# Performance work log

Measured on AMD Instinct MI355X. Metric: run time of the kernel, lower is better.

The kernel has to match this reference:

```python
import jax, jax.numpy as jnp
import numpy as np

N, D, C = 8192, 128, 64
LAMBDA = 0.25
DELTA = 1.0


def setup_inputs() -> dict:
    key = jax.random.key(0)
    k1, k2, k3 = jax.random.split(key, 3)
    out = jax.random.normal(k1, (N, C), dtype=jnp.float32)
    feat = jax.random.normal(k2, (N, D), dtype=jnp.float32)
    y = jax.random.randint(k3, (N,), 0, C)
    return {"out": out, "feat": feat, "y": y}


def reference(out, feat, y):
    n = feat.shape[0]
    # Per-class matrices: zeroing rows not in class c leaves singular values
    # identical to slicing X[y==c] (extra zero rows only add zero singular
    # directions), so one batched SVD over [C, N, D] replaces the CPU loop.
    masks = (y[None, :] == jnp.arange(C)[:, None]).astype(feat.dtype)  # [C, N]
    Xc = feat[None, :, :] * masks[:, :, None]                           # [C, N, D]
    Sc = jnp.linalg.svd(Xc, compute_uv=False)                           # [C, min(N,D)]
    obj_c = jnp.maximum(Sc.sum(-1), DELTA).sum()                        # sum_c max(||X_c||_*, DELTA)
    S_all = jnp.linalg.svd(feat, compute_uv=False)
    ole = (obj_c - S_all.sum()) / n * LAMBDA
    # Cross entropy (mean reduction, matching nn.CrossEntropyLoss)
    logp = jax.nn.log_softmax(out, axis=-1)
    xe = -jnp.take_along_axis(logp, y[:, None], axis=1).mean()
    loss = ole + xe
    return jnp.reshape(loss, (1,))  # torch returns shape-[1] tensor
```

## Files before the change

### kernel.cpp

```cpp
#include <hip/hip_runtime.h>
#include <math.h>


#define N_ROWS 8192
#define DIM    128
#define NCLS   64
#define NITER  7
#define EPSN   2e-4f
#define LAMBDA_ 0.25f
#define DELTA_  1.0f
#define MAGIC  0x13579BDF

typedef __attribute__((ext_vector_type(8))) short s16x8;
typedef __attribute__((ext_vector_type(4))) short s16x4;
typedef __attribute__((ext_vector_type(4))) float f32x4;

static __device__ const float NS_C1[NITER] =
  {2.554408f, 2.491084f, 2.189178f, 2.050122f, 1.686417f, 1.5f, 1.5f};
static __device__ const float NS_C2[NITER] =
  {2.469261f, 2.290137f, 1.554316f, 1.276543f, 0.710544f, 0.5f, 0.5f};

__device__ __forceinline__ unsigned short f2bf(float f) {
  unsigned u = __float_as_uint(f);
  u = (u + 0x7FFFu + ((u >> 16) & 1u)) >> 16;
  return (unsigned short)u;
}
__device__ __forceinline__ float bf2f(unsigned short h) {
  return __uint_as_float(((unsigned)h) << 16);
}

__device__ __forceinline__ int swz_idx(int i, int j) {
  return i * 128 + (((j >> 3) ^ (i & 15)) << 3) + (j & 7);
}

__device__ __forceinline__ s16x8 load_frag(const short* buf, int row0,
                                           int kstep, int lane) {
  int m  = row0 + (lane & 15);
  int kg = kstep * 4 + (lane >> 4);
  return *(const s16x8*)(buf + m * 128 + ((kg ^ (m & 15)) << 3));
}

__device__ __forceinline__ void flag_set(int* p) {
  __threadfence();
  __hip_atomic_store(p, MAGIC, __ATOMIC_RELEASE, __HIP_MEMORY_SCOPE_AGENT);
}
__device__ __forceinline__ void flag_wait(const int* p) {
  while (__hip_atomic_load(p, __ATOMIC_ACQUIRE, __HIP_MEMORY_SCOPE_AGENT) != MAGIC)
    __builtin_amdgcn_s_sleep(8);
}

__global__ __launch_bounds__(512, 1) void ole_fused(const float* __restrict__ feat,
                                                    const int* __restrict__ y,
                                                    const float* __restrict__ logits,
                                                    float* __restrict__ Gall,
                                                    float* __restrict__ nuc,
                                                    float* __restrict__ cepart,
                                                    int* __restrict__ flags,
                                                    float* __restrict__ out) {
  int* gramdone = flags;
  int* nflag    = flags + NCLS;
  int* ceflag   = flags + 2 * NCLS;

  __shared__ __align__(16) short Yb[DIM * DIM];
  __shared__ __align__(16) short Mh[DIM * DIM];
  __shared__ __align__(16) short Ml[DIM * DIM];
  __shared__ __align__(16) short Zb[DIM * DIM];
  __shared__ int cnt;

  const int bid  = blockIdx.x;
  const int tid  = threadIdx.x;
  const int lane = tid & 63;
  const int quad = lane >> 4;
  const int wv   = tid >> 6;

  if (bid > NCLS) {
    const int gwave = (bid - NCLS - 1) * 8 + wv;
    float acc = 0.f;
    for (int row = gwave; row < N_ROWS; row += 512) {
      float v = logits[row * NCLS + lane];
      float mx = v;
      for (int off = 32; off > 0; off >>= 1) mx = fmaxf(mx, __shfl_xor(mx, off, 64));
      float e = expf(v - mx);
      for (int off = 32; off > 0; off >>= 1) e += __shfl_xor(e, off, 64);
      if (lane == 0) {
        int t = y[row];
        acc += (mx + logf(e)) - logits[row * NCLS + t];
      }
    }
    if (lane == 0) cepart[gwave] = acc;
    __syncthreads();
    if (tid == 0) flag_set(&ceflag[bid - NCLS - 1]);
    return;
  }

  const int ti = tid >> 5, tj = tid & 31;
  const int i0 = ti * 8,  j0 = tj * 4;

  float  accg[8][4];
  float4 gs[8];
  float tpart = 0.f, fpart = 0.f;

  if (bid < NCLS) {
    int* list = (int*)Yb;
    float (*xs)[DIM] = (float (*)[DIM])Mh;

    if (tid == 0) cnt = 0;
    __syncthreads();
    const int4* y4 = (const int4*)y;
#pragma unroll
    for (int t = 0; t < 4; ++t) {
      int g4 = tid + 512 * t;
      int4 v = y4[g4];
      int r0 = g4 * 4;
      if (v.x == bid) list[atomicAdd(&cnt, 1)] = r0;
      if (v.y == bid) list[atomicAdd(&cnt, 1)] = r0 + 1;
      if (v.z == bid) list[atomicAdd(&cnt, 1)] = r0 + 2;
      if (v.w == bid) list[atomicAdd(&cnt, 1)] = r0 + 3;
    }
    __syncthreads();
    const int n = cnt;

#pragma unroll
    for (int a = 0; a < 8; ++a)
#pragma unroll
      for (int b = 0; b < 4; ++b) accg[a][b] = 0.f;

    for (int base = 0; base < n; base += 16) {
      int li = base + ti;
      float4 v = make_float4(0.f, 0.f, 0.f, 0.f);
      if (li < n) v = *(const float4*)(feat + (size_t)list[li] * DIM + j0);
      __syncthreads();
      *(float4*)(&xs[ti][j0]) = v;
      __syncthreads();
#pragma unroll
      for (int rw = 0; rw < 16; ++rw) {
        float xi[8], xj[4];
#pragma unroll
        for (int a = 0; a < 8; ++a) xi[a] = xs[rw][i0 + a];
#pragma unroll
        for (int b = 0; b < 4; ++b) xj[b] = xs[rw][j0 + b];
#pragma unroll
        for (int a = 0; a < 8; ++a)
#pragma unroll
          for (int b = 0; b < 4; ++b) accg[a][b] = fmaf(xi[a], xj[b], accg[a][b]);
      }
    }

#pragma unroll
    for (int a = 0; a < 8; ++a)
#pragma unroll
      for (int b = 0; b < 4; ++b) {
        float g = accg[a][b];
        atomicAdd(&Gall[(i0 + a) * DIM + (j0 + b)], g);
        fpart += g * g;
        if (i0 + a == j0 + b) tpart += g;
      }
    __syncthreads();
    if (tid == 0) flag_set(&gramdone[bid]);
  } else {
    if (tid < NCLS) flag_wait(&gramdone[tid]);
    __syncthreads();
    const float4* Gm4 = (const float4*)Gall;
#pragma unroll
    for (int t = 0; t < 8; ++t) {
      int idx4 = tid + 512 * t;
      float4 v = Gm4[idx4];
      gs[t] = v;
      fpart += v.x * v.x + v.y * v.y + v.z * v.z + v.w * v.w;
      int flat = idx4 * 4, i = flat >> 7, jj = flat & 127;
      if (jj <= i && i < jj + 4) tpart += ((const float*)&v)[i - jj];
    }
  }

  for (int off = 32; off > 0; off >>= 1) {
    tpart += __shfl_down(tpart, off, 64);
    fpart += __shfl_down(fpart, off, 64);
  }
  float* redf = (float*)Zb;
  if (lane == 0) { redf[wv] = tpart; redf[8 + wv] = fpart; }
  __syncthreads();
  float trace = 0.f, fro2 = 0.f;
#pragma unroll
  for (int w = 0; w < 8; ++w) { trace += redf[w]; fro2 += redf[8 + w]; }
  __syncthreads();

  float s = sqrtf(fro2);
  if (s < 1e-12f) s = 1.f;
  const float invs = 1.f / s;
  const float eps  = EPSN * trace * invs;

  if (bid < NCLS) {
#pragma unroll
    for (int a = 0; a < 8; ++a) {
      int i = i0 + a;
      s16x4 vh;
#pragma unroll
      for (int b = 0; b < 4; ++b) {
        float x = accg[a][b] * invs + ((i == j0 + b) ? eps : 0.f);
        vh[b] = (short)f2bf(x);
      }
      *(s16x4*)(Yb + swz_idx(i, j0)) = vh;
    }
  } else {
#pragma unroll
    for (int t = 0; t < 8; ++t) {
      int idx4 = tid + 512 * t;
      int flat = idx4 * 4, i = flat >> 7, jj = flat & 127;
      s16x4 vh;
#pragma unroll
      for (int e = 0; e < 4; ++e) {
        float x = ((const float*)&gs[t])[e] * invs + ((i == jj + e) ? eps : 0.f);
        vh[e] = (short)f2bf(x);
      }
      *(s16x4*)(Yb + swz_idx(i, jj)) = vh;
    }
  }
  for (int grp = tid; grp < DIM * 16; grp += 512) {
    int i = grp >> 4, g = grp & 15;
    s16x8 v = (s16x8)0;
    if ((i >> 3) == g) v[i & 7] = (short)0x3F80;
    *(s16x8*)(Zb + i * 128 + ((g ^ (i & 15)) << 3)) = v;
  }
  __syncthreads();

  const int wr = wv >> 2;
  const int wc = wv & 3;

  for (int it = 0; it < NITER; ++it) {
    const float kA = NS_C1[it];
    const float kB = NS_C2[it];

    f32x4 acc[4][2];
#pragma unroll
    for (int r = 0; r < 4; ++r)
#pragma unroll
      for (int c2 = 0; c2 < 2; ++c2) acc[r][c2] = (f32x4)0.f;
#pragma unroll
    for (int ks = 0; ks < 4; ++ks) {
      s16x8 a[4], b[2];
#pragma unroll
      for (int r = 0; r < 4; ++r) a[r] = load_frag(Zb, (4 * wr + r) * 16, ks, lane);
#pragma unroll
      for (int c2 = 0; c2 < 2; ++c2) b[c2] = load_frag(Yb, (2 * wc + c2) * 16, ks, lane);
#pragma unroll
      for (int r = 0; r < 4; ++r)
#pragma unroll
        for (int c2 = 0; c2 < 2; ++c2)
          acc[r][c2] = __builtin_amdgcn_mfma_f32_16x16x32_bf16(a[r], b[c2], acc[r][c2], 0, 0, 0);
    }
#pragma unroll
    for (int r = 0; r < 4; ++r) {
      int ibase = (4 * wr + r) * 16 + quad * 4;
      int cg    = ibase >> 3;
#pragma unroll
      for (int c2 = 0; c2 < 2; ++c2) {
        int jg  = (2 * wc + c2) * 16 + (lane & 15);
        int idx = jg * 128 + ((cg ^ (jg & 15)) << 3) + (ibase & 7);
        s16x4 vh, vl;
#pragma unroll
        for (int e = 0; e < 4; ++e) {
          float mv = -kB * acc[r][c2][e] + ((ibase + e == jg) ? kA : 0.f);
          mv = fminf(fmaxf(mv, -4.f), 4.f);
          unsigned short hh = f2bf(mv);
          vh[e] = (short)hh;
          vl[e] = (short)f2bf(mv - bf2f(hh));
        }
        *(s16x4*)(Mh + idx) = vh;
        *(s16x4*)(Ml + idx) = vl;
      }
    }
    __syncthreads();

    f32x4 ay[4][2], az[4][2];
#pragma unroll
    for (int r = 0; r < 4; ++r)
#pragma unroll
      for (int c2 = 0; c2 < 2; ++c2) { ay[r][c2] = (f32x4)0.f; az[r][c2] = (f32x4)0.f; }
#pragma unroll
    for (int ks = 0; ks < 4; ++ks) {
      s16x8 aMh[4], aMl[4], bY[2], bZ[2];
#pragma unroll
      for (int r = 0; r < 4; ++r) {
        int rb = (4 * wr + r) * 16;
        aMh[r] = load_frag(Mh, rb, ks, lane);
        aMl[r] = load_frag(Ml, rb, ks, lane);
      }
#pragma unroll
      for (int c2 = 0; c2 < 2; ++c2) {
        int cb = (2 * wc + c2) * 16;
        bY[c2] = load_frag(Yb, cb, ks, lane);
        bZ[c2] = load_frag(Zb, cb, ks, lane);
      }
#pragma unroll
      for (int r = 0; r < 4; ++r)
#pragma unroll
        for (int c2 = 0; c2 < 2; ++c2) {
          ay[r][c2] = __builtin_amdgcn_mfma_f32_16x16x32_bf16(aMh[r], bY[c2], ay[r][c2], 0, 0, 0);
          ay[r][c2] = __builtin_amdgcn_mfma_f32_16x16x32_bf16(aMl[r], bY[c2], ay[r][c2], 0, 0, 0);
          az[r][c2] = __builtin_amdgcn_mfma_f32_16x16x32_bf16(aMh[r], bZ[c2], az[r][c2], 0, 0, 0);
          az[r][c2] = __builtin_amdgcn_mfma_f32_16x16x32_bf16(aMl[r], bZ[c2], az[r][c2], 0, 0, 0);
        }
    }
    __syncthreads();

#pragma unroll
    for (int r = 0; r < 4; ++r) {
      int ibase = (4 * wr + r) * 16 + quad * 4;
      int cg    = ibase >> 3;
#pragma unroll
      for (int c2 = 0; c2 < 2; ++c2) {
        int jg  = (2 * wc + c2) * 16 + (lane & 15);
        int idx = jg * 128 + ((cg ^ (jg & 15)) << 3) + (ibase & 7);
        s16x4 vy, vz;
#pragma unroll
        for (int e = 0; e < 4; ++e) {
          vy[e] = (short)f2bf(ay[r][c2][e]);
          vz[e] = (short)f2bf(az[r][c2][e]);
        }
        *(s16x4*)(Yb + idx) = vy;
        *(s16x4*)(Zb + idx) = vz;
      }
    }
    __syncthreads();
  }

  float t_gz = 0.f, t_z = 0.f, t_z3 = 0.f;
  if (bid < NCLS) {
#pragma unroll
    for (int a = 0; a < 8; ++a) {
      s16x4 zv = *(const s16x4*)(Zb + swz_idx(i0 + a, j0));
#pragma unroll
      for (int b = 0; b < 4; ++b) t_gz += accg[a][b] * bf2f((unsigned short)zv[b]);
    }
  } else {
#pragma unroll
    for (int t = 0; t < 8; ++t) {
      int idx4 = tid + 512 * t;
      int flat = idx4 * 4, i = flat >> 7, jj = flat & 127;
      s16x4 zv = *(const s16x4*)(Zb + swz_idx(i, jj));
#pragma unroll
      for (int e = 0; e < 4; ++e) t_gz += ((const float*)&gs[t])[e] * bf2f((unsigned short)zv[e]);
    }
  }
  if (tid < DIM) t_z = bf2f((unsigned short)Zb[swz_idx(tid, tid)]);

  {
    f32x4 u[4][2];
#pragma unroll
    for (int r = 0; r < 4; ++r)
#pragma unroll
      for (int c2 = 0; c2 < 2; ++c2) u[r][c2] = (f32x4)0.f;
#pragma unroll
    for (int ks = 0; ks < 4; ++ks) {
      s16x8 a[4], b[2];
#pragma unroll
      for (int r = 0; r < 4; ++r) a[r] = load_frag(Zb, (4 * wr + r) * 16, ks, lane);
#pragma unroll
      for (int c2 = 0; c2 < 2; ++c2) b[c2] = load_frag(Zb, (2 * wc + c2) * 16, ks, lane);
#pragma unroll
      for (int r = 0; r < 4; ++r)
#pragma unroll
        for (int c2 = 0; c2 < 2; ++c2)
          u[r][c2] = __builtin_amdgcn_mfma_f32_16x16x32_bf16(a[r], b[c2], u[r][c2], 0, 0, 0);
    }
#pragma unroll
    for (int r = 0; r < 4; ++r) {
      int ibase = (4 * wr + r) * 16 + quad * 4;
      int cg    = ibase >> 3;
#pragma unroll
      for (int c2 = 0; c2 < 2; ++c2) {
        int jg  = (2 * wc + c2) * 16 + (lane & 15);
        int idx = jg * 128 + ((cg ^ (jg & 15)) << 3) + (ibase & 7);
        s16x4 zt = *(const s16x4*)(Zb + idx);
#pragma unroll
        for (int e = 0; e < 4; ++e) t_z3 += u[r][c2][e] * bf2f((unsigned short)zt[e]);
      }
    }
  }

  for (int off = 32; off > 0; off >>= 1) {
    t_gz += __shfl_down(t_gz, off, 64);
    t_z  += __shfl_down(t_z,  off, 64);
    t_z3 += __shfl_down(t_z3, off, 64);
  }
  __syncthreads();
  float* red = (float*)Mh;
  if (lane == 0) { red[wv] = t_gz; red[8 + wv] = t_z; red[16 + wv] = t_z3; }
  __syncthreads();

  float nuc_own = 0.f;
  if (tid == 0) {
    float gz = 0.f, z1 = 0.f, z3 = 0.f;
#pragma unroll
    for (int w = 0; w < 8; ++w) { gz += red[w]; z1 += red[8 + w]; z3 += red[16 + w]; }
    float trsq = gz * invs + 0.5f * eps * z1 - 0.125f * eps * eps * z3;
    nuc_own = sqrtf(s) * trsq;
    nuc[bid] = nuc_own;
  }

  if (bid < NCLS) {
    if (tid == 0) flag_set(&nflag[bid]);
    return;
  }

  if (tid < NCLS)          flag_wait(&nflag[tid]);
  else if (tid < 2 * NCLS) flag_wait(&ceflag[tid - NCLS]);
  __syncthreads();

  float ce2 = cepart[tid];
  float vmx = (tid < NCLS) ? fmaxf(nuc[tid], DELTA_) : 0.f;
  for (int off = 32; off > 0; off >>= 1) {
    vmx += __shfl_down(vmx, off, 64);
    ce2 += __shfl_down(ce2, off, 64);
  }
  if (lane == 0) { red[wv] = vmx; red[8 + wv] = ce2; }
  __syncthreads();
  if (tid == 0) {
    float vs = 0.f, cs = 0.f;
#pragma unroll
    for (int w = 0; w < 8; ++w) { vs += red[w]; cs += red[8 + w]; }
    float ole = (vs - nuc_own) * (LAMBDA_ / (float)N_ROWS);
    out[0] = ole + cs / (float)N_ROWS;
  }
}

extern "C" void kernel_launch(void* const* d_in, const int* in_sizes, int n_in,
                              void* d_out, int out_size, void* d_ws, size_t ws_size,
                              hipStream_t stream) {
  const float* logits = (const float*)d_in[0];
  const float* feat   = (const float*)d_in[1];
  const int*   yp     = (const int*)d_in[2];

  float* Gall   = (float*)d_ws;
  int*   flags  = (int*)(Gall + DIM * DIM);
  float* nuc    = (float*)(flags + 192);
  float* cepart = nuc + 68;

  hipMemsetAsync(d_ws, 0, (DIM * DIM + 192) * sizeof(float), stream);

  ole_fused<<<2 * NCLS + 1, 512, 0, stream>>>(feat, yp, logits, Gall, nuc,
                                              cepart, flags, (float*)d_out);
}
```

Measured before the change: 132.8 us.

## Store per-class Grams in workspace, reduce with dedicated blocks, use 1024-thread blocks

```diff
diff --git a/kernel.cpp b/kernel.cpp
--- a/kernel.cpp
+++ b/kernel.cpp
@@ -5,6 +5,8 @@
 #define N_ROWS 8192
 #define DIM    128
 #define NCLS   64
+#define NB_CE  64
+#define NB_BLD 16
 #define NITER  7
 #define EPSN   2e-4f
 #define LAMBDA_ 0.25f
@@ -49,17 +51,33 @@
     __builtin_amdgcn_s_sleep(8);
 }
 
-__global__ __launch_bounds__(512, 1) void ole_fused(const float* __restrict__ feat,
-                                                    const int* __restrict__ y,
-                                                    const float* __restrict__ logits,
-                                                    float* __restrict__ Gall,
-                                                    float* __restrict__ nuc,
-                                                    float* __restrict__ cepart,
-                                                    int* __restrict__ flags,
-                                                    float* __restrict__ out) {
+__device__ __forceinline__ void gram_row(const float* __restrict__ feat,
+                                         int row, int i0, int j0,
+                                         float accg[4][4]) {
+  const float* fr = feat + (size_t)row * DIM;
+  float4 xi = *(const float4*)(fr + i0);
+  float4 xj = *(const float4*)(fr + j0);
+  const float* xip = (const float*)&xi;
+  const float* xjp = (const float*)&xj;
+#pragma unroll
+  for (int a = 0; a < 4; ++a)
+#pragma unroll
+    for (int b = 0; b < 4; ++b)
+      accg[a][b] = fmaf(xip[a], xjp[b], accg[a][b]);
+}
+
+__global__ __launch_bounds__(1024, 1) void ole_fused(const float* __restrict__ feat,
+                                                     const int* __restrict__ y,
+                                                     const float* __restrict__ logits,
+                                                     float* __restrict__ G,
+                                                     float* __restrict__ nuc,
+                                                     float* __restrict__ cepart,
+                                                     int* __restrict__ flags,
+                                                     float* __restrict__ out) {
   int* gramdone = flags;
-  int* nflag    = flags + NCLS;
-  int* ceflag   = flags + 2 * NCLS;
+  int* gallf    = flags + 64;
+  int* nflag    = flags + 80;
+  int* ceflag   = flags + 144;
 
   __shared__ __align__(16) short Yb[DIM * DIM];
   __shared__ __align__(16) short Mh[DIM * DIM];
@@ -73,10 +91,12 @@
   const int quad = lane >> 4;
   const int wv   = tid >> 6;
 
-  if (bid > NCLS) {
-    const int gwave = (bid - NCLS - 1) * 8 + wv;
+  float* Gall = G + (size_t)NCLS * DIM * DIM;
+
+  if (bid > NCLS && bid <= NCLS + NB_CE) {
+    const int gwave = (bid - NCLS - 1) * 16 + wv;
     float acc = 0.f;
-    for (int row = gwave; row < N_ROWS; row += 512) {
+    for (int row = gwave; row < N_ROWS; row += 1024) {
       float v = logits[row * NCLS + lane];
       float mx = v;
       for (int off = 32; off > 0; off >>= 1) mx = fmaxf(mx, __shfl_xor(mx, off, 64));
@@ -93,23 +113,53 @@
     return;
   }
 
+  if (bid > NCLS + NB_CE) {
+    const int gb = bid - (NCLS + 1 + NB_CE);
+    if (tid < NCLS) flag_wait(&gramdone[tid]);
+    __syncthreads();
+    const float4* G4 = (const float4*)G;
+    float4* bsum = (float4*)Yb;
+    {
+      const int pos = tid & 255, grp = tid >> 8;
+      const int idx4 = gb * 256 + pos;
+      float4 s = make_float4(0.f, 0.f, 0.f, 0.f);
+#pragma unroll 4
+      for (int c = grp * 16; c < grp * 16 + 16; ++c) {
+        float4 v = G4[(size_t)c * (DIM * DIM / 4) + idx4];
+        s.x += v.x; s.y += v.y; s.z += v.z; s.w += v.w;
+      }
+      bsum[tid] = s;
+    }
+    __syncthreads();
+    if (tid < 256) {
+      float4 s = bsum[tid];
+#pragma unroll
+      for (int g = 1; g < 4; ++g) {
+        float4 v = bsum[g * 256 + tid];
+        s.x += v.x; s.y += v.y; s.z += v.z; s.w += v.w;
+      }
+      ((float4*)Gall)[gb * 256 + tid] = s;
+    }
+    __syncthreads();
+    if (tid == 0) flag_set(&gallf[gb]);
+    return;
+  }
+
   const int ti = tid >> 5, tj = tid & 31;
-  const int i0 = ti * 8,  j0 = tj * 4;
-
-  float  accg[8][4];
-  float4 gs[8];
+  const int i0 = ti * 4,  j0 = tj * 4;
+
   float tpart = 0.f, fpart = 0.f;
+  float4 gs[4];
+  float  accg[4][4];
 
   if (bid < NCLS) {
     int* list = (int*)Yb;
-    float (*xs)[DIM] = (float (*)[DIM])Mh;
-
     if (tid == 0) cnt = 0;
     __syncthreads();
     const int4* y4 = (const int4*)y;
 #pragma unroll
-    for (int t = 0; t < 4; ++t) {
-      int g4 = tid + 512 * t;
+    for (int t = 0; t < 2; ++t) {
+      int g4 = tid + 1024 * t;
       int4 v = y4[g4];
       int r0 = g4 * 4;
       if (v.x == bid) list[atomicAdd(&cnt, 1)] = r0;
@@ -121,49 +171,43 @@
     const int n = cnt;
 
 #pragma unroll
-    for (int a = 0; a < 8; ++a)
+    for (int a = 0; a < 4; ++a)
 #pragma unroll
       for (int b = 0; b < 4; ++b) accg[a][b] = 0.f;
 
-    for (int base = 0; base < n; base += 16) {
-      int li = base + ti;
-      float4 v = make_float4(0.f, 0.f, 0.f, 0.f);
-      if (li < n) v = *(const float4*)(feat + (size_t)list[li] * DIM + j0);
-      __syncthreads();
-      *(float4*)(&xs[ti][j0]) = v;
-      __syncthreads();
-#pragma unroll
-      for (int rw = 0; rw < 16; ++rw) {
-        float xi[8], xj[4];
-#pragma unroll
-        for (int a = 0; a < 8; ++a) xi[a] = xs[rw][i0 + a];
-#pragma unroll
-        for (int b = 0; b < 4; ++b) xj[b] = xs[rw][j0 + b];
-#pragma unroll
-        for (int a = 0; a < 8; ++a)
-#pragma unroll
-          for (int b = 0; b < 4; ++b) accg[a][b] = fmaf(xi[a], xj[b], accg[a][b]);
-      }
-    }
-
-#pragma unroll
-    for (int a = 0; a < 8; ++a)
+    int r = 0;
+    for (; r + 4 <= n; r += 4) {
+      int4 rw4 = *(const int4*)(list + r);
+      gram_row(feat, rw4.x, i0, j0, accg);
+      gram_row(feat, rw4.y, i0, j0, accg);
+      gram_row(feat, rw4.z, i0, j0, accg);
+      gram_row(feat, rw4.w, i0, j0, accg);
+    }
+    for (; r < n; ++r) gram_row(feat, list[r], i0, j0, accg);
+
+    float* Gc = G + (size_t)bid * DIM * DIM;
+#pragma unroll
+    for (int a = 0; a < 4; ++a) {
+      float4 row;
+      float* rp = (float*)&row;
 #pragma unroll
       for (int b = 0; b < 4; ++b) {
         float g = accg[a][b];
-        atomicAdd(&Gall[(i0 + a) * DIM + (j0 + b)], g);
+        rp[b] = g;
         fpart += g * g;
         if (i0 + a == j0 + b) tpart += g;
       }
+      *(float4*)(Gc + (size_t)(i0 + a) * DIM + j0) = row;
+    }
     __syncthreads();
     if (tid == 0) flag_set(&gramdone[bid]);
   } else {
-    if (tid < NCLS) flag_wait(&gramdone[tid]);
+    if (tid < NB_BLD) flag_wait(&gallf[tid]);
     __syncthreads();
     const float4* Gm4 = (const float4*)Gall;
 #pragma unroll
-    for (int t = 0; t < 8; ++t) {
-      int idx4 = tid + 512 * t;
+    for (int t = 0; t < 4; ++t) {
+      int idx4 = tid + 1024 * t;
       float4 v = Gm4[idx4];
       gs[t] = v;
       fpart += v.x * v.x + v.y * v.y + v.z * v.z + v.w * v.w;
@@ -177,11 +221,11 @@
     fpart += __shfl_down(fpart, off, 64);
   }
   float* redf = (float*)Zb;
-  if (lane == 0) { redf[wv] = tpart; redf[8 + wv] = fpart; }
+  if (lane == 0) { redf[wv] = tpart; redf[16 + wv] = fpart; }
   __syncthreads();
   float trace = 0.f, fro2 = 0.f;
 #pragma unroll
-  for (int w = 0; w < 8; ++w) { trace += redf[w]; fro2 += redf[8 + w]; }
+  for (int w = 0; w < 16; ++w) { trace += redf[w]; fro2 += redf[16 + w]; }
   __syncthreads();
 
   float s = sqrtf(fro2);
@@ -191,7 +235,7 @@
 
   if (bid < NCLS) {
 #pragma unroll
-    for (int a = 0; a < 8; ++a) {
+    for (int a = 0; a < 4; ++a) {
       int i = i0 + a;
       s16x4 vh;
 #pragma unroll
@@ -203,8 +247,8 @@
     }
   } else {
 #pragma unroll
-    for (int t = 0; t < 8; ++t) {
-      int idx4 = tid + 512 * t;
+    for (int t = 0; t < 4; ++t) {
+      int idx4 = tid + 1024 * t;
       int flat = idx4 * 4, i = flat >> 7, jj = flat & 127;
       s16x4 vh;
 #pragma unroll
@@ -215,7 +259,7 @@
       *(s16x4*)(Yb + swz_idx(i, jj)) = vh;
     }
   }
-  for (int grp = tid; grp < DIM * 16; grp += 512) {
+  for (int grp = tid; grp < DIM * 16; grp += 1024) {
     int i = grp >> 4, g = grp & 15;
     s16x8 v = (s16x8)0;
     if ((i >> 3) == g) v[i & 7] = (short)0x3F80;
@@ -230,27 +274,27 @@
     const float kA = NS_C1[it];
     const float kB = NS_C2[it];
 
-    f32x4 acc[4][2];
-#pragma unroll
-    for (int r = 0; r < 4; ++r)
+    f32x4 acc[2][2];
+#pragma unroll
+    for (int r = 0; r < 2; ++r)
 #pragma unroll
       for (int c2 = 0; c2 < 2; ++c2) acc[r][c2] = (f32x4)0.f;
 #pragma unroll
     for (int ks = 0; ks < 4; ++ks) {
-      s16x8 a[4], b[2];
-#pragma unroll
-      for (int r = 0; r < 4; ++r) a[r] = load_frag(Zb, (4 * wr + r) * 16, ks, lane);
+      s16x8 a[2], b[2];
+#pragma unroll
+      for (int r = 0; r < 2; ++r) a[r] = load_frag(Zb, (2 * wr + r) * 16, ks, lane);
 #pragma unroll
       for (int c2 = 0; c2 < 2; ++c2) b[c2] = load_frag(Yb, (2 * wc + c2) * 16, ks, lane);
 #pragma unroll
-      for (int r = 0; r < 4; ++r)
+      for (int r = 0; r < 2; ++r)
 #pragma unroll
         for (int c2 = 0; c2 < 2; ++c2)
           acc[r][c2] = __builtin_amdgcn_mfma_f32_16x16x32_bf16(a[r], b[c2], acc[r][c2], 0, 0, 0);
     }
 #pragma unroll
-    for (int r = 0; r < 4; ++r) {
-      int ibase = (4 * wr + r) * 16 + quad * 4;
+    for (int r = 0; r < 2; ++r) {
+      int ibase = (2 * wr + r) * 16 + quad * 4;
       int cg    = ibase >> 3;
 #pragma unroll
       for (int c2 = 0; c2 < 2; ++c2) {
@@ -271,17 +315,17 @@
     }
     __syncthreads();
 
-    f32x4 ay[4][2], az[4][2];
-#pragma unroll
-    for (int r = 0; r < 4; ++r)
+    f32x4 ay[2][2], az[2][2];
+#pragma unroll
+    for (int r = 0; r < 2; ++r)
 #pragma unroll
       for (int c2 = 0; c2 < 2; ++c2) { ay[r][c2] = (f32x4)0.f; az[r][c2] = (f32x4)0.f; }
 #pragma unroll
     for (int ks = 0; ks < 4; ++ks) {
-      s16x8 aMh[4], aMl[4], bY[2], bZ[2];
-#pragma unroll
-      for (int r = 0; r < 4; ++r) {
-        int rb = (4 * wr + r) * 16;
+      s16x8 aMh[2], aMl[2], bY[2], bZ[2];
+#pragma unroll
+      for (int r = 0; r < 2; ++r) {
+        int rb = (2 * wr + r) * 16;
         aMh[r] = load_frag(Mh, rb, ks, lane);
         aMl[r] = load_frag(Ml, rb, ks, lane);
       }
@@ -292,7 +336,7 @@
         bZ[c2] = load_frag(Zb, cb, ks, lane);
       }
 #pragma unroll
-      for (int r = 0; r < 4; ++r)
+      for (int r = 0; r < 2; ++r)
 #pragma unroll
         for (int c2 = 0; c2 < 2; ++c2) {
           ay[r][c2] = __builtin_amdgcn_mfma_f32_16x16x32_bf16(aMh[r], bY[c2], ay[r][c2], 0, 0, 0);
@@ -304,8 +348,8 @@
     __syncthreads();
 
 #pragma unroll
-    for (int r = 0; r < 4; ++r) {
-      int ibase = (4 * wr + r) * 16 + quad * 4;
+    for (int r = 0; r < 2; ++r) {
+      int ibase = (2 * wr + r) * 16 + quad * 4;
       int cg    = ibase >> 3;
 #pragma unroll
       for (int c2 = 0; c2 < 2; ++c2) {
@@ -325,47 +369,42 @@
   }
 
   float t_gz = 0.f, t_z = 0.f, t_z3 = 0.f;
-  if (bid < NCLS) {
-#pragma unroll
-    for (int a = 0; a < 8; ++a) {
-      s16x4 zv = *(const s16x4*)(Zb + swz_idx(i0 + a, j0));
-#pragma unroll
-      for (int b = 0; b < 4; ++b) t_gz += accg[a][b] * bf2f((unsigned short)zv[b]);
-    }
-  } else {
-#pragma unroll
-    for (int t = 0; t < 8; ++t) {
-      int idx4 = tid + 512 * t;
-      int flat = idx4 * 4, i = flat >> 7, jj = flat & 127;
-      s16x4 zv = *(const s16x4*)(Zb + swz_idx(i, jj));
-#pragma unroll
-      for (int e = 0; e < 4; ++e) t_gz += ((const float*)&gs[t])[e] * bf2f((unsigned short)zv[e]);
+  {
+    const float* Ganc = G + (size_t)bid * DIM * DIM;
+#pragma unroll
+    for (int a = 0; a < 4; ++a) {
+      int i = i0 + a;
+      float4 gv = *(const float4*)(Ganc + (size_t)i * DIM + j0);
+      s16x4 zv = *(const s16x4*)(Zb + swz_idx(i, j0));
+#pragma unroll
+      for (int b = 0; b < 4; ++b)
+        t_gz += ((const float*)&gv)[b] * bf2f((unsigned short)zv[b]);
     }
   }
   if (tid < DIM) t_z = bf2f((unsigned short)Zb[swz_idx(tid, tid)]);
 
   {
-    f32x4 u[4][2];
-#pragma unroll
-    for (int r = 0; r < 4; ++r)
+    f32x4 u[2][2];
+#pragma unroll
+    for (int r = 0; r < 2; ++r)
 #pragma unroll
       for (int c2 = 0; c2 < 2; ++c2) u[r][c2] = (f32x4)0.f;
 #pragma unroll
     for (int ks = 0; ks < 4; ++ks) {
-      s16x8 a[4], b[2];
-#pragma unroll
-      for (int r = 0; r < 4; ++r) a[r] = load_frag(Zb, (4 * wr + r) * 16, ks, lane);
+      s16x8 a[2], b[2];
+#pragma unroll
+      for (int r = 0; r < 2; ++r) a[r] = load_frag(Zb, (2 * wr + r) * 16, ks, lane);
 #pragma unroll
       for (int c2 = 0; c2 < 2; ++c2) b[c2] = load_frag(Zb, (2 * wc + c2) * 16, ks, lane);
 #pragma unroll
-      for (int r = 0; r < 4; ++r)
+      for (int r = 0; r < 2; ++r)
 #pragma unroll
         for (int c2 = 0; c2 < 2; ++c2)
           u[r][c2] = __builtin_amdgcn_mfma_f32_16x16x32_bf16(a[r], b[c2], u[r][c2], 0, 0, 0);
     }
 #pragma unroll
-    for (int r = 0; r < 4; ++r) {
-      int ibase = (4 * wr + r) * 16 + quad * 4;
+    for (int r = 0; r < 2; ++r) {
+      int ibase = (2 * wr + r) * 16 + quad * 4;
       int cg    = ibase >> 3;
 #pragma unroll
       for (int c2 = 0; c2 < 2; ++c2) {
@@ -385,14 +424,14 @@
   }
   __syncthreads();
   float* red = (float*)Mh;
-  if (lane == 0) { red[wv] = t_gz; red[8 + wv] = t_z; red[16 + wv] = t_z3; }
+  if (lane == 0) { red[wv] = t_gz; red[16 + wv] = t_z; red[32 + wv] = t_z3; }
   __syncthreads();
 
   float nuc_own = 0.f;
   if (tid == 0) {
     float gz = 0.f, z1 = 0.f, z3 = 0.f;
 #pragma unroll
-    for (int w = 0; w < 8; ++w) { gz += red[w]; z1 += red[8 + w]; z3 += red[16 + w]; }
+    for (int w = 0; w < 16; ++w) { gz += red[w]; z1 += red[16 + w]; z3 += red[32 + w]; }
     float trsq = gz * invs + 0.5f * eps * z1 - 0.125f * eps * eps * z3;
     nuc_own = sqrtf(s) * trsq;
     nuc[bid] = nuc_own;
@@ -413,12 +452,12 @@
     vmx += __shfl_down(vmx, off, 64);
     ce2 += __shfl_down(ce2, off, 64);
   }
-  if (lane == 0) { red[wv] = vmx; red[8 + wv] = ce2; }
+  if (lane == 0) { red[wv] = vmx; red[16 + wv] = ce2; }
   __syncthreads();
   if (tid == 0) {
     float vs = 0.f, cs = 0.f;
 #pragma unroll
-    for (int w = 0; w < 8; ++w) { vs += red[w]; cs += red[8 + w]; }
+    for (int w = 0; w < 16; ++w) { vs += red[w]; cs += red[16 + w]; }
     float ole = (vs - nuc_own) * (LAMBDA_ / (float)N_ROWS);
     out[0] = ole + cs / (float)N_ROWS;
   }
@@ -431,13 +470,13 @@
   const float* feat   = (const float*)d_in[1];
   const int*   yp     = (const int*)d_in[2];
 
-  float* Gall   = (float*)d_ws;
-  int*   flags  = (int*)(Gall + DIM * DIM);
-  float* nuc    = (float*)(flags + 192);
+  int*   flags  = (int*)d_ws;
+  float* nuc    = (float*)d_ws + 256;
   float* cepart = nuc + 68;
-
-  hipMemsetAsync(d_ws, 0, (DIM * DIM + 192) * sizeof(float), stream);
-
-  ole_fused<<<2 * NCLS + 1, 512, 0, stream>>>(feat, yp, logits, Gall, nuc,
-                                              cepart, flags, (float*)d_out);
-}
+  float* G      = cepart + 1024;
+
+  hipMemsetAsync(d_ws, 0, 256 * sizeof(int), stream);
+
+  ole_fused<<<NCLS + 1 + NB_CE + NB_BLD, 1024, 0, stream>>>(
+      feat, yp, logits, G, nuc, cepart, flags, (float*)d_out);
+}
```

New measurement: 147.2 us. +10.9%, slower.

## Replace atomic Gram accumulation with per-class stores and parallel reduction blocks

Applied to the files above, without the earlier changes.

```diff
diff --git a/kernel.cpp b/kernel.cpp
--- a/kernel.cpp
+++ b/kernel.cpp
@@ -5,6 +5,8 @@
 #define N_ROWS 8192
 #define DIM    128
 #define NCLS   64
+#define NB_CE  64
+#define NB_BLD 16
 #define NITER  7
 #define EPSN   2e-4f
 #define LAMBDA_ 0.25f
@@ -52,14 +54,15 @@
 __global__ __launch_bounds__(512, 1) void ole_fused(const float* __restrict__ feat,
                                                     const int* __restrict__ y,
                                                     const float* __restrict__ logits,
-                                                    float* __restrict__ Gall,
+                                                    float* __restrict__ G,
                                                     float* __restrict__ nuc,
                                                     float* __restrict__ cepart,
                                                     int* __restrict__ flags,
                                                     float* __restrict__ out) {
   int* gramdone = flags;
-  int* nflag    = flags + NCLS;
-  int* ceflag   = flags + 2 * NCLS;
+  int* gallf    = flags + 64;
+  int* nflag    = flags + 80;
+  int* ceflag   = flags + 144;
 
   __shared__ __align__(16) short Yb[DIM * DIM];
   __shared__ __align__(16) short Mh[DIM * DIM];
@@ -73,7 +76,9 @@
   const int quad = lane >> 4;
   const int wv   = tid >> 6;
 
-  if (bid > NCLS) {
+  float* Gall = G + (size_t)NCLS * DIM * DIM;
+
+  if (bid > NCLS && bid <= NCLS + NB_CE) {
     const int gwave = (bid - NCLS - 1) * 8 + wv;
     float acc = 0.f;
     for (int row = gwave; row < N_ROWS; row += 512) {
@@ -93,32 +98,54 @@
     return;
   }
 
+  if (bid > NCLS + NB_CE) {
+    const int gb = bid - (NCLS + 1 + NB_CE);
+    if (tid < NCLS) flag_wait(&gramdone[tid]);
+    __syncthreads();
+    if (tid < 256) {
+      const int idx4 = gb * 256 + tid;
+      const float4* G4 = (const float4*)G;
+      float4 s = make_float4(0.f, 0.f, 0.f, 0.f);
+#pragma unroll 8
+      for (int c = 0; c < NCLS; ++c) {
+        float4 v = G4[(size_t)c * (DIM * DIM / 4) + idx4];
+        s.x += v.x; s.y += v.y; s.z += v.z; s.w += v.w;
+      }
+      ((float4*)Gall)[idx4] = s;
+    }
+    __syncthreads();
+    if (tid == 0) flag_set(&gallf[gb]);
+    return;
+  }
+
   const int ti = tid >> 5, tj = tid & 31;
   const int i0 = ti * 8,  j0 = tj * 4;
 
+  float tpart = 0.f, fpart = 0.f;
+  float4 gs[8];
   float  accg[8][4];
-  float4 gs[8];
-  float tpart = 0.f, fpart = 0.f;
 
   if (bid < NCLS) {
     int* list = (int*)Yb;
+    if (tid == 0) cnt = 0;
+    __syncthreads();
+#pragma unroll
+    for (int t = 0; t < 16; ++t) {
+      int row = t * 512 + tid;
+      bool hit = (y[row] == bid);
+      unsigned long long m = __ballot(hit);
+      int base = 0;
+      if (lane == 0 && m) base = atomicAdd(&cnt, __popcll(m));
+      base = __shfl(base, 0, 64);
+      if (hit) {
+        int pre = __popcll(m & ((1ull << lane) - 1ull));
+        list[base + pre] = row;
+      }
+    }
+    __syncthreads();
+    const int n = cnt;
+
     float (*xs)[DIM] = (float (*)[DIM])Mh;
-
-    if (tid == 0) cnt = 0;
-    __syncthreads();
-    const int4* y4 = (const int4*)y;
-#pragma unroll
-    for (int t = 0; t < 4; ++t) {
-      int g4 = tid + 512 * t;
-      int4 v = y4[g4];
-      int r0 = g4 * 4;
-      if (v.x == bid) list[atomicAdd(&cnt, 1)] = r0;
-      if (v.y == bid) list[atomicAdd(&cnt, 1)] = r0 + 1;
-      if (v.z == bid) list[atomicAdd(&cnt, 1)] = r0 + 2;
-      if (v.w == bid) list[atomicAdd(&cnt, 1)] = r0 + 3;
-    }
-    __syncthreads();
-    const int n = cnt;
 
 #pragma unroll
     for (int a = 0; a < 8; ++a)
@@ -146,19 +173,24 @@
       }
     }
 
-#pragma unroll
-    for (int a = 0; a < 8; ++a)
+    float* Gc = G + (size_t)bid * DIM * DIM;
+#pragma unroll
+    for (int a = 0; a < 8; ++a) {
+      float4 row;
+      float* rp = (float*)&row;
 #pragma unroll
       for (int b = 0; b < 4; ++b) {
         float g = accg[a][b];
-        atomicAdd(&Gall[(i0 + a) * DIM + (j0 + b)], g);
+        rp[b] = g;
         fpart += g * g;
         if (i0 + a == j0 + b) tpart += g;
       }
+      *(float4*)(Gc + (size_t)(i0 + a) * DIM + j0) = row;
+    }
     __syncthreads();
     if (tid == 0) flag_set(&gramdone[bid]);
   } else {
-    if (tid < NCLS) flag_wait(&gramdone[tid]);
+    if (tid < NB_BLD) flag_wait(&gallf[tid]);
     __syncthreads();
     const float4* Gm4 = (const float4*)Gall;
 #pragma unroll
@@ -431,13 +463,13 @@
   const float* feat   = (const float*)d_in[1];
   const int*   yp     = (const int*)d_in[2];
 
-  float* Gall   = (float*)d_ws;
-  int*   flags  = (int*)(Gall + DIM * DIM);
-  float* nuc    = (float*)(flags + 192);
+  int*   flags  = (int*)d_ws;
+  float* nuc    = (float*)d_ws + 256;
   float* cepart = nuc + 68;
-
-  hipMemsetAsync(d_ws, 0, (DIM * DIM + 192) * sizeof(float), stream);
-
-  ole_fused<<<2 * NCLS + 1, 512, 0, stream>>>(feat, yp, logits, Gall, nuc,
-                                              cepart, flags, (float*)d_out);
-}
+  float* G      = cepart + 512;
+
+  hipMemsetAsync(d_ws, 0, 256 * sizeof(int), stream);
+
+  ole_fused<<<NCLS + 1 + NB_CE + NB_BLD, 512, 0, stream>>>(
+      feat, yp, logits, G, nuc, cepart, flags, (float*)d_out);
+}
```

Result: no change. 133.1 us (+0.3%).
